# Kernel tuning notes

Measured on AMD Instinct MI355X. Metric: run time of the kernel, lower is better.

## Reference

```python
import jax, jax.numpy as jnp
import numpy as np

B, ORDER, S, D, H = 64, 2, 256, 256, 8
HD = D // H  # head_dim = 32


def setup_inputs() -> dict:
    key = jax.random.key(0)
    ks = jax.random.split(key, 6)
    stdv = 1.0 / np.sqrt(HD)
    return {
        "x": jax.random.normal(ks[0], (B, ORDER, S, D), jnp.float32),
        "A": jax.random.randint(ks[1], (B, ORDER, S, S), 0, 5, jnp.int32),
        # params stacked as [order, conv(1|2), ...]
        "Wp": jax.random.normal(ks[2], (ORDER, 2, D, D), jnp.float32) * stdv,
        "bp": jnp.zeros((ORDER, 2, D), jnp.float32),
        "att_src": jax.random.normal(ks[3], (ORDER, 2, H, HD), jnp.float32) * stdv,
        "att_dst": jax.random.normal(ks[4], (ORDER, 2, H, HD), jnp.float32) * stdv,
        "gbias": jnp.zeros((ORDER, 2, D), jnp.float32),
        "prelu_a": 0.25 * jnp.ones((D,), jnp.float32),
    }


def _gat(x, edge, W, b, a_src, a_dst, gb):
    """Dense additive GAT over a [B,S,S] boolean adjacency. Eval mode (dropout inert)."""
    Bt, St, Dt = x.shape
    x = x @ W + b                                   # project (bias=True)
    xh = x.reshape(Bt, St, H, HD)
    a_s = jnp.einsum('bshd,hd->bsh', xh, a_src)     # per-source score
    a_d = jnp.einsum('bthd,hd->bth', xh, a_dst)     # per-dest score
    alpha = a_s[:, :, None, :] + a_d[:, None, :, :]  # [B, S_src, S_dst, H]
    alpha = jnp.where(edge[..., None], alpha, 0.0)   # masked_fill((A != 1), 0)
    alpha = jnp.where(alpha >= 0, alpha, 0.2 * alpha)  # leaky_relu(0.2)
    alpha = jax.nn.softmax(alpha, axis=1)            # stable softmax over source axis
    out = jnp.einsum('bsth,bshd->bthd', alpha, xh).reshape(Bt, St, Dt)
    return out + x + gb                              # add_self_loops + bias


def reference(x, A, Wp, bp, att_src, att_dst, gbias, prelu_a):
    # A1 = (A==2)+(A==4); A2 = (A==3)+(A==4); edge iff value == 1
    A1 = (A == 2) | (A == 4)
    A2 = (A == 3) | (A == 4)
    hs = []
    for i in range(ORDER):  # order is a small structural constant (=2)
        h1 = _gat(x[:, i], A1[:, i], Wp[i, 0], bp[i, 0], att_src[i, 0], att_dst[i, 0], gbias[i, 0])
        h2 = _gat(x[:, i], A2[:, i], Wp[i, 1], bp[i, 1], att_src[i, 1], att_dst[i, 1], gbias[i, 1])
        hs.append(h1 + h2)
    h = jnp.stack(hs, axis=1)                       # [B, order, S, D]
    out = h + h.mean(axis=1, keepdims=True)
    out = jnp.where(out >= 0, out, prelu_a * out)   # PReLU(dim)
    return out
```

## Files before the change

### kernel.cpp

```cpp
#include <hip/hip_runtime.h>
#include <hip/hip_bf16.h>
#include <math.h>

typedef __bf16 bf16;
typedef __bf16 bf16x4 __attribute__((ext_vector_type(4)));
typedef __bf16 bf16x8 __attribute__((ext_vector_type(8)));
typedef float f32x4 __attribute__((ext_vector_type(4)));
typedef unsigned int u32;

#define LOG2E 1.44269504f

__device__ inline float fast_exp2(float x) {
#if __has_builtin(__builtin_amdgcn_exp2f)
    return __builtin_amdgcn_exp2f(x);
#else
    return exp2f(x);
#endif
}

#define GL2LDS(gp, lp) __builtin_amdgcn_global_load_lds( \
    (const __attribute__((address_space(1))) u32*)(gp),  \
    (__attribute__((address_space(3))) u32*)(lp), 16, 0, 0)


__global__ void prep_k(const float* __restrict__ x, const float* __restrict__ Wp,
                       const int* __restrict__ A, bf16* __restrict__ xb,
                       bf16* __restrict__ Wt, unsigned* __restrict__ m1,
                       unsigned* __restrict__ m2) {
    int bid = blockIdx.x;
    int tid = threadIdx.x;
    if (bid < 4096) {
        int gid = bid * 256 + tid;
        const f32x4* xp = (const f32x4*)x + (size_t)gid * 2;
        f32x4 a = xp[0], b4 = xp[1];
        bf16x8 o;
#pragma unroll
        for (int c = 0; c < 4; ++c) { o[c] = (bf16)a[c]; o[c + 4] = (bf16)b4[c]; }
        ((bf16x8*)xb)[gid] = o;
    } else if (bid < 5120) {
        int gid = (bid - 4096) * 256 + tid;
        int k = gid & 255;
        int n = (gid >> 8) & 255;
        int ij = gid >> 16;
        Wt[gid] = (bf16)Wp[(ij * 256 + k) * 256 + n];
    } else {
        int pb = bid - 5120;
        int sh = pb & 1;
        int ijb = pb >> 1;
        const int* Ab = A + ((size_t)ijb << 16);
        unsigned w1 = 0, w2 = 0;
#pragma unroll 8
        for (int sl = 0; sl < 128; ++sl) {
            int s = sh * 128 + sl;
            int av = Ab[s * 256 + tid];
            unsigned f1 = (av == 2 || av == 4) ? 1u : 0u;
            unsigned f2 = (av == 3 || av == 4) ? 1u : 0u;
            w1 |= f1 << (s & 31);
            w2 |= f2 << (s & 31);
            if ((s & 31) == 31) {
                int kc = s >> 5;
                m1[(ijb * 8 + kc) * 256 + tid] = w1;
                m2[(ijb * 8 + kc) * 256 + tid] = w2;
                w1 = 0; w2 = 0;
            }
        }
    }
}

__launch_bounds__(256)
__global__ void proj_gemm(const bf16* __restrict__ xb, const bf16* __restrict__ Wt,
                          const float* __restrict__ bp, const float* __restrict__ att_src,
                          const float* __restrict__ att_dst, bf16* __restrict__ Vt,
                          float* __restrict__ asb, float* __restrict__ adb) {
    __shared__ char smem[35840 + 1024];
    bf16* As = (bf16*)smem;
    bf16* Bs = (bf16*)(smem + 8192);
    bf16* TL = (bf16*)smem;
    float* attL = (float*)(smem + 35840);

    int tid = threadIdx.x;
    int mt = blockIdx.x, nt = blockIdx.y, i = blockIdx.z;
    int n0 = nt * 128;
    int j = n0 >> 8, d0 = n0 & 255;
    int ij = i * 2 + j;
    int m0 = mt * 128;
    int b = m0 >> 8, shalf = (m0 >> 7) & 1;

    {
        int which = tid >> 7, rest = tid & 127;
        const float* ap = which ? att_dst : att_src;
        attL[tid] = ap[(ij * 8 + (d0 >> 5) + (rest >> 5)) * 32 + (rest & 31)];
    }

    int c0 = tid, c1 = tid + 256;
    int r0 = c0 >> 2, k80 = (c0 & 3) * 8;
    int r1 = c1 >> 2, k81 = (c1 & 3) * 8;
    const bf16* ga0 = xb + (((size_t)((b * 2 + i) * 256 + shalf * 128 + r0)) << 8) + k80;
    const bf16* ga1 = xb + (((size_t)((b * 2 + i) * 256 + shalf * 128 + r1)) << 8) + k81;
    const bf16* gb0 = Wt + (((size_t)(ij * 256 + d0 + r0)) << 8) + k80;
    const bf16* gb1 = Wt + (((size_t)(ij * 256 + d0 + r1)) << 8) + k81;
    bf16* la0 = As + c0 * 8;
    bf16* la1 = As + c1 * 8;
    bf16* lb0 = Bs + c0 * 8;
    bf16* lb1 = Bs + c1 * 8;

    int wave = tid >> 6, lane = tid & 63;
    int wd = (wave & 1) * 64, ws = (wave >> 1) * 64;
    int lrow = lane & 15, quad = lane >> 4;

    f32x4 acc[4][4];
#pragma unroll
    for (int a = 0; a < 4; ++a)
#pragma unroll
        for (int c = 0; c < 4; ++c) acc[a][c] = (f32x4){0.f, 0.f, 0.f, 0.f};

    for (int kc = 0; kc < 8; ++kc) {
        int k0 = kc * 32;
        GL2LDS(ga0 + k0, la0);
        GL2LDS(ga1 + k0, la1);
        GL2LDS(gb0 + k0, lb0);
        GL2LDS(gb1 + k0, lb1);
        __syncthreads();
        bf16x8 wf[4], xf[4];
#pragma unroll
        for (int dj = 0; dj < 4; ++dj)
            wf[dj] = *(const bf16x8*)&Bs[(wd + dj * 16 + lrow) * 32 + quad * 8];
#pragma unroll
        for (int sj = 0; sj < 4; ++sj)
            xf[sj] = *(const bf16x8*)&As[(ws + sj * 16 + lrow) * 32 + quad * 8];
#pragma unroll
        for (int dj = 0; dj < 4; ++dj)
#pragma unroll
            for (int sj = 0; sj < 4; ++sj)
                acc[dj][sj] = __builtin_amdgcn_mfma_f32_16x16x32_bf16(wf[dj], xf[sj], acc[dj][sj], 0, 0, 0);
        __syncthreads();
    }

    float sc[2][2][4];
#pragma unroll
    for (int w2 = 0; w2 < 2; ++w2)
#pragma unroll
        for (int hf = 0; hf < 2; ++hf)
#pragma unroll
            for (int sj = 0; sj < 4; ++sj) sc[w2][hf][sj] = 0.f;
#pragma unroll
    for (int dj = 0; dj < 4; ++dj) {
        int hf = dj >> 1;
#pragma unroll
        for (int r = 0; r < 4; ++r) {
            int dl = wd + dj * 16 + quad * 4 + r;
            float bias = bp[ij * 256 + d0 + dl];
            float avs = attL[dl];
            float avd = attL[128 + dl];
#pragma unroll
            for (int sj = 0; sj < 4; ++sj) {
                float v = acc[dj][sj][r] + bias;
                TL[dl * 140 + ws + sj * 16 + lrow] = (bf16)v;
                sc[0][hf][sj] += v * avs;
                sc[1][hf][sj] += v * avd;
            }
        }
    }
#pragma unroll
    for (int w2 = 0; w2 < 2; ++w2)
#pragma unroll
        for (int hf = 0; hf < 2; ++hf)
#pragma unroll
            for (int sj = 0; sj < 4; ++sj) {
                float v = sc[w2][hf][sj];
                v += __shfl_xor(v, 16, 64);
                v += __shfl_xor(v, 32, 64);
                sc[w2][hf][sj] = v;
            }
    if (lane < 16) {
        int hbase = (d0 >> 5) + (wd >> 5);
#pragma unroll
        for (int w2 = 0; w2 < 2; ++w2) {
            float* outp = w2 ? adb : asb;
#pragma unroll
            for (int hf = 0; hf < 2; ++hf) {
                int hh = hbase + hf;
#pragma unroll
                for (int sj = 0; sj < 4; ++sj) {
                    int s = ws + sj * 16 + lane;
                    outp[((ij * 64 + b) * 8 + hh) * 256 + shalf * 128 + s] = sc[w2][hf][sj] * LOG2E;
                }
            }
        }
    }
    __syncthreads();

    {
        int dl = tid >> 1, sh64 = (tid & 1) * 64;
        const bf16* src = TL + dl * 140 + sh64;
        bf16* dst = Vt + (((size_t)(ij * 64 + b)) << 16) + (size_t)(d0 + dl) * 256
                    + shalf * 128 + sh64;
#pragma unroll
        for (int q = 0; q < 16; ++q)
            *(bf16x4*)(dst + q * 4) = *(const bf16x4*)(src + q * 4);
    }
}

__launch_bounds__(256, 3)
__global__ void attn_k(const bf16* __restrict__ Vt, const unsigned* __restrict__ m1,
                       const unsigned* __restrict__ m2, const float* __restrict__ asb,
                       const float* __restrict__ adb, const float* __restrict__ gbias,
                       const float* __restrict__ prelu_a, float* __restrict__ out) {
    int bid = blockIdx.x;
    int tt = bid & 7, hg = (bid >> 3) & 1, b = bid >> 4;
    int t0 = tt * 32;
    int tid = threadIdx.x, wave = tid >> 6, lane = tid & 63;
    int lrow = lane & 15, quad = lane >> 4;
    int h = hg * 4 + wave;

    __shared__ float    as_l[2][2][4][256];
    __shared__ unsigned ml[2][2][8][32];
    __shared__ float    l_lds[2][2][4][32];

#pragma unroll
    for (int p = 0; p < 16; ++p) {
        int idx = p * 256 + tid;
        int i = idx >> 11, c = (idx >> 10) & 1, w = (idx >> 8) & 3, s = idx & 255;
        as_l[i][c][w][s] = asb[(((i * 2 + c) * 64 + b) * 8 + hg * 4 + w) * 256 + s];
    }
#pragma unroll
    for (int p = 0; p < 4; ++p) {
        int idx = p * 256 + tid;
        int i = idx >> 9, c = (idx >> 8) & 1, kc = (idx >> 5) & 7, tl = idx & 31;
        ml[i][c][kc][tl] = (c ? m2 : m1)[((b * 2 + i) * 8 + kc) * 256 + t0 + tl];
    }
    float ad_r[2][2][2];
#pragma unroll
    for (int i = 0; i < 2; ++i)
#pragma unroll
        for (int c = 0; c < 2; ++c)
#pragma unroll
            for (int mi = 0; mi < 2; ++mi)
                ad_r[i][c][mi] = adb[(((i * 2 + c) * 64 + b) * 8 + h) * 256 + t0 + mi * 16 + lrow];
    __syncthreads();

    const bf16* vtp[2][2];
#pragma unroll
    for (int i = 0; i < 2; ++i)
#pragma unroll
        for (int c = 0; c < 2; ++c)
            vtp[i][c] = Vt + (((size_t)(((i * 2 + c) * 64 + b) * 8 + h)) << 13);

    f32x4 acc[2][2][2][2];
#pragma unroll
    for (int i = 0; i < 2; ++i)
#pragma unroll
        for (int c = 0; c < 2; ++c)
#pragma unroll
            for (int mi = 0; mi < 2; ++mi)
#pragma unroll
                for (int ni = 0; ni < 2; ++ni) acc[i][c][mi][ni] = (f32x4){0.f, 0.f, 0.f, 0.f};
    float lsum[2][2][2];
#pragma unroll
    for (int i = 0; i < 2; ++i)
#pragma unroll
        for (int c = 0; c < 2; ++c)
#pragma unroll
            for (int mi = 0; mi < 2; ++mi) lsum[i][c][mi] = 0.f;

    for (int kc = 0; kc < 8; ++kc) {
        int s0 = kc * 32;
        bf16x8 bfr[2][2][2];
#pragma unroll
        for (int i = 0; i < 2; ++i)
#pragma unroll
            for (int c = 0; c < 2; ++c)
#pragma unroll
                for (int ni = 0; ni < 2; ++ni)
                    bfr[i][c][ni] = *(const bf16x8*)(vtp[i][c] + (size_t)(ni * 16 + lrow) * 256 + s0 + quad * 8);
#pragma unroll
        for (int i = 0; i < 2; ++i) {
#pragma unroll
            for (int c = 0; c < 2; ++c) {
                f32x4 asv0 = *(const f32x4*)&as_l[i][c][wave][s0 + quad * 8];
                f32x4 asv1 = *(const f32x4*)&as_l[i][c][wave][s0 + quad * 8 + 4];
#pragma unroll
                for (int mi = 0; mi < 2; ++mi) {
                    unsigned wb = ml[i][c][kc][mi * 16 + lrow] >> (quad * 8);
                    float ad = ad_r[i][c][mi];
                    bf16x8 af;
#pragma unroll
                    for (int j = 0; j < 8; ++j) {
                        float u = (j < 4 ? asv0[j] : asv1[j - 4]) + ad;
                        u = fmaxf(u, 0.2f * u);
                        u = ((wb >> j) & 1u) ? u : 0.f;
                        float e = fast_exp2(u);
                        lsum[i][c][mi] += e;
                        af[j] = (bf16)e;
                    }
                    acc[i][c][mi][0] = __builtin_amdgcn_mfma_f32_16x16x32_bf16(af, bfr[i][c][0], acc[i][c][mi][0], 0, 0, 0);
                    acc[i][c][mi][1] = __builtin_amdgcn_mfma_f32_16x16x32_bf16(af, bfr[i][c][1], acc[i][c][mi][1], 0, 0, 0);
                }
            }
        }
    }

#pragma unroll
    for (int i = 0; i < 2; ++i)
#pragma unroll
        for (int c = 0; c < 2; ++c)
#pragma unroll
            for (int mi = 0; mi < 2; ++mi) {
                float l = lsum[i][c][mi];
                l += __shfl_xor(l, 16, 64);
                l += __shfl_xor(l, 32, 64);
                if (lane < 16) l_lds[i][c][wave][mi * 16 + lane] = l;
            }
    __syncthreads();

#pragma unroll
    for (int ni = 0; ni < 2; ++ni) {
        int dcol = h * 32 + ni * 16 + lrow;
        float gb0 = gbias[0 * 256 + dcol] + gbias[1 * 256 + dcol];
        float gb1 = gbias[2 * 256 + dcol] + gbias[3 * 256 + dcol];
        float pa = prelu_a[dcol];
        const bf16* r00 = vtp[0][0] + (size_t)(ni * 16 + lrow) * 256 + t0;
        const bf16* r01 = vtp[0][1] + (size_t)(ni * 16 + lrow) * 256 + t0;
        const bf16* r10 = vtp[1][0] + (size_t)(ni * 16 + lrow) * 256 + t0;
        const bf16* r11 = vtp[1][1] + (size_t)(ni * 16 + lrow) * 256 + t0;
#pragma unroll
        for (int mi = 0; mi < 2; ++mi) {
            bf16x4 rv00 = *(const bf16x4*)(r00 + mi * 16 + quad * 4);
            bf16x4 rv01 = *(const bf16x4*)(r01 + mi * 16 + quad * 4);
            bf16x4 rv10 = *(const bf16x4*)(r10 + mi * 16 + quad * 4);
            bf16x4 rv11 = *(const bf16x4*)(r11 + mi * 16 + quad * 4);
#pragma unroll
            for (int r = 0; r < 4; ++r) {
                int tl = mi * 16 + quad * 4 + r;
                int t = t0 + tl;
                float v0 = acc[0][0][mi][ni][r] * __builtin_amdgcn_rcpf(l_lds[0][0][wave][tl])
                         + acc[0][1][mi][ni][r] * __builtin_amdgcn_rcpf(l_lds[0][1][wave][tl])
                         + (float)rv00[r] + (float)rv01[r] + gb0;
                float v1 = acc[1][0][mi][ni][r] * __builtin_amdgcn_rcpf(l_lds[1][0][wave][tl])
                         + acc[1][1][mi][ni][r] * __builtin_amdgcn_rcpf(l_lds[1][1][wave][tl])
                         + (float)rv10[r] + (float)rv11[r] + gb1;
                float mn = 0.5f * (v0 + v1);
                float a0 = v0 + mn, a1 = v1 + mn;
                a0 = a0 >= 0.f ? a0 : pa * a0;
                a1 = a1 >= 0.f ? a1 : pa * a1;
                out[(((size_t)((b * 2 + 0) * 256 + t)) << 8) + dcol] = a0;
                out[(((size_t)((b * 2 + 1) * 256 + t)) << 8) + dcol] = a1;
            }
        }
    }
}

extern "C" void kernel_launch(void* const* d_in, const int* in_sizes, int n_in,
                              void* d_out, int out_size, void* d_ws, size_t ws_size,
                              hipStream_t stream) {
    const float* x       = (const float*)d_in[0];
    const int*   A       = (const int*)d_in[1];
    const float* Wp      = (const float*)d_in[2];
    const float* bp      = (const float*)d_in[3];
    const float* att_src = (const float*)d_in[4];
    const float* att_dst = (const float*)d_in[5];
    const float* gbias   = (const float*)d_in[6];
    const float* prelu_a = (const float*)d_in[7];
    float* out = (float*)d_out;

    char* ws = (char*)d_ws;
    bf16*     Wt  = (bf16*)ws;
    unsigned* m1  = (unsigned*)(ws + 524288);
    unsigned* m2  = (unsigned*)(ws + 1572864);
    float*    asb = (float*)(ws + 2621440);
    float*    adb = (float*)(ws + 4718592);
    bf16*     xb  = (bf16*)(ws + 6815744);
    bf16*     Vt  = (bf16*)(ws + 23592960);

    prep_k<<<5376, 256, 0, stream>>>(x, Wp, A, xb, Wt, m1, m2);
    dim3 gproj(128, 4, 2);
    proj_gemm<<<gproj, 256, 0, stream>>>(xb, Wt, bp, att_src, att_dst, Vt, asb, adb);
    attn_k<<<1024, 256, 0, stream>>>(Vt, m1, m2, asb, adb, gbias, prelu_a, out);
}
```

Baseline: 231.8 us.

## Fuse fp32-to-bf16 conversion of x into projection GEMM and rebalance prep

```diff
diff --git a/kernel.cpp b/kernel.cpp
--- a/kernel.cpp
+++ b/kernel.cpp
@@ -23,58 +23,45 @@
     (__attribute__((address_space(3))) u32*)(lp), 16, 0, 0)
 
 
-__global__ void prep_k(const float* __restrict__ x, const float* __restrict__ Wp,
-                       const int* __restrict__ A, bf16* __restrict__ xb,
+__global__ void prep_k(const float* __restrict__ Wp, const int* __restrict__ A,
                        bf16* __restrict__ Wt, unsigned* __restrict__ m1,
                        unsigned* __restrict__ m2) {
     int bid = blockIdx.x;
     int tid = threadIdx.x;
-    if (bid < 4096) {
+    if (bid < 1024) {
         int gid = bid * 256 + tid;
-        const f32x4* xp = (const f32x4*)x + (size_t)gid * 2;
-        f32x4 a = xp[0], b4 = xp[1];
-        bf16x8 o;
-#pragma unroll
-        for (int c = 0; c < 4; ++c) { o[c] = (bf16)a[c]; o[c + 4] = (bf16)b4[c]; }
-        ((bf16x8*)xb)[gid] = o;
-    } else if (bid < 5120) {
-        int gid = (bid - 4096) * 256 + tid;
         int k = gid & 255;
         int n = (gid >> 8) & 255;
         int ij = gid >> 16;
         Wt[gid] = (bf16)Wp[(ij * 256 + k) * 256 + n];
     } else {
-        int pb = bid - 5120;
-        int sh = pb & 1;
-        int ijb = pb >> 1;
+        int pb = bid - 1024;
+        int kc = pb & 7;
+        int ijb = pb >> 3;
         const int* Ab = A + ((size_t)ijb << 16);
         unsigned w1 = 0, w2 = 0;
-#pragma unroll 8
-        for (int sl = 0; sl < 128; ++sl) {
-            int s = sh * 128 + sl;
+#pragma unroll
+        for (int sl = 0; sl < 32; ++sl) {
+            int s = kc * 32 + sl;
             int av = Ab[s * 256 + tid];
             unsigned f1 = (av == 2 || av == 4) ? 1u : 0u;
             unsigned f2 = (av == 3 || av == 4) ? 1u : 0u;
-            w1 |= f1 << (s & 31);
-            w2 |= f2 << (s & 31);
-            if ((s & 31) == 31) {
-                int kc = s >> 5;
-                m1[(ijb * 8 + kc) * 256 + tid] = w1;
-                m2[(ijb * 8 + kc) * 256 + tid] = w2;
-                w1 = 0; w2 = 0;
-            }
-        }
+            w1 |= f1 << sl;
+            w2 |= f2 << sl;
+        }
+        m1[(ijb * 8 + kc) * 256 + tid] = w1;
+        m2[(ijb * 8 + kc) * 256 + tid] = w2;
     }
 }
 
 __launch_bounds__(256)
-__global__ void proj_gemm(const bf16* __restrict__ xb, const bf16* __restrict__ Wt,
+__global__ void proj_gemm(const float* __restrict__ x, const bf16* __restrict__ Wt,
                           const float* __restrict__ bp, const float* __restrict__ att_src,
                           const float* __restrict__ att_dst, bf16* __restrict__ Vt,
                           float* __restrict__ asb, float* __restrict__ adb) {
     __shared__ char smem[35840 + 1024];
     bf16* As = (bf16*)smem;
-    bf16* Bs = (bf16*)(smem + 8192);
+    bf16* Bs = (bf16*)(smem + 10240);
     bf16* TL = (bf16*)smem;
     float* attL = (float*)(smem + 35840);
 
@@ -92,15 +79,11 @@
         attL[tid] = ap[(ij * 8 + (d0 >> 5) + (rest >> 5)) * 32 + (rest & 31)];
     }
 
+    int mr = tid >> 1, kq = (tid & 1) * 16;
+    const float* xrow = x + (((size_t)((b * 2 + i) * 256 + shalf * 128 + mr)) << 8) + kq;
     int c0 = tid, c1 = tid + 256;
-    int r0 = c0 >> 2, k80 = (c0 & 3) * 8;
-    int r1 = c1 >> 2, k81 = (c1 & 3) * 8;
-    const bf16* ga0 = xb + (((size_t)((b * 2 + i) * 256 + shalf * 128 + r0)) << 8) + k80;
-    const bf16* ga1 = xb + (((size_t)((b * 2 + i) * 256 + shalf * 128 + r1)) << 8) + k81;
-    const bf16* gb0 = Wt + (((size_t)(ij * 256 + d0 + r0)) << 8) + k80;
-    const bf16* gb1 = Wt + (((size_t)(ij * 256 + d0 + r1)) << 8) + k81;
-    bf16* la0 = As + c0 * 8;
-    bf16* la1 = As + c1 * 8;
+    const bf16* gb0 = Wt + (((size_t)(ij * 256 + d0 + (c0 >> 2))) << 8) + (c0 & 3) * 8;
+    const bf16* gb1 = Wt + (((size_t)(ij * 256 + d0 + (c1 >> 2))) << 8) + (c1 & 3) * 8;
     bf16* lb0 = Bs + c0 * 8;
     bf16* lb1 = Bs + c1 * 8;
 
@@ -116,10 +99,23 @@
 
     for (int kc = 0; kc < 8; ++kc) {
         int k0 = kc * 32;
-        GL2LDS(ga0 + k0, la0);
-        GL2LDS(ga1 + k0, la1);
         GL2LDS(gb0 + k0, lb0);
         GL2LDS(gb1 + k0, lb1);
+        {
+            const float* ap = xrow + k0;
+            f32x4 xa0 = *(const f32x4*)(ap);
+            f32x4 xa1 = *(const f32x4*)(ap + 4);
+            f32x4 xa2 = *(const f32x4*)(ap + 8);
+            f32x4 xa3 = *(const f32x4*)(ap + 12);
+            bf16x8 w0, w1;
+#pragma unroll
+            for (int q = 0; q < 4; ++q) {
+                w0[q] = (bf16)xa0[q]; w0[q + 4] = (bf16)xa1[q];
+                w1[q] = (bf16)xa2[q]; w1[q + 4] = (bf16)xa3[q];
+            }
+            *(bf16x8*)&As[mr * 40 + kq]     = w0;
+            *(bf16x8*)&As[mr * 40 + kq + 8] = w1;
+        }
         __syncthreads();
         bf16x8 wf[4], xf[4];
 #pragma unroll
@@ -127,7 +123,7 @@
             wf[dj] = *(const bf16x8*)&Bs[(wd + dj * 16 + lrow) * 32 + quad * 8];
 #pragma unroll
         for (int sj = 0; sj < 4; ++sj)
-            xf[sj] = *(const bf16x8*)&As[(ws + sj * 16 + lrow) * 32 + quad * 8];
+            xf[sj] = *(const bf16x8*)&As[(ws + sj * 16 + lrow) * 40 + quad * 8];
 #pragma unroll
         for (int dj = 0; dj < 4; ++dj)
 #pragma unroll
@@ -207,7 +203,9 @@
                        const float* __restrict__ adb, const float* __restrict__ gbias,
                        const float* __restrict__ prelu_a, float* __restrict__ out) {
     int bid = blockIdx.x;
-    int tt = bid & 7, hg = (bid >> 3) & 1, b = bid >> 4;
+    int blow = bid & 7;
+    int rest = bid >> 3;
+    int tt = rest & 7, hg = (rest >> 3) & 1, b = (rest >> 4) * 8 + blow;
     int t0 = tt * 32;
     int tid = threadIdx.x, wave = tid >> 6, lane = tid & 63;
     int lrow = lane & 15, quad = lane >> 4;
@@ -369,11 +367,10 @@
     unsigned* m2  = (unsigned*)(ws + 1572864);
     float*    asb = (float*)(ws + 2621440);
     float*    adb = (float*)(ws + 4718592);
-    bf16*     xb  = (bf16*)(ws + 6815744);
-    bf16*     Vt  = (bf16*)(ws + 23592960);
-
-    prep_k<<<5376, 256, 0, stream>>>(x, Wp, A, xb, Wt, m1, m2);
+    bf16*     Vt  = (bf16*)(ws + 6815744);
+
+    prep_k<<<2048, 256, 0, stream>>>(Wp, A, Wt, m1, m2);
     dim3 gproj(128, 4, 2);
-    proj_gemm<<<gproj, 256, 0, stream>>>(xb, Wt, bp, att_src, att_dst, Vt, asb, adb);
+    proj_gemm<<<gproj, 256, 0, stream>>>(x, Wt, bp, att_src, att_dst, Vt, asb, adb);
     attn_k<<<1024, 256, 0, stream>>>(Vt, m1, m2, asb, adb, gbias, prelu_a, out);
 }
```

Result: faster. 191.5 us (-17.4%).
